# Kernel optimization log

Measured on AMD Instinct MI355X. Metric: run time of the kernel, lower is better.

The kernel has to match this reference:

```python
import jax, jax.numpy as jnp
import numpy as np

N = 2048   # num_nodes
D = 64     # dim
B = 256    # batch of queried nodes
TAU = 1.0


def setup_inputs() -> dict:
    key = jax.random.key(0)
    k_w, k_idx, k_ctx = jax.random.split(key, 3)
    limit = np.sqrt(2.0 / (2 * N)).astype(np.float32)
    W = jax.random.normal(k_w, (N, N, D), dtype=jnp.float32) * limit
    node_indices = jax.random.randint(k_idx, (B,), 0, N, dtype=jnp.int64)
    context_vector = jax.random.normal(k_ctx, (D,), dtype=jnp.float32)
    return {"node_indices": node_indices, "context_vector": context_vector, "W": W}


def reference(node_indices, context_vector, W):
    # Gather per-node weight slabs: (B, N, D)
    w_ij = W[node_indices]
    # Contract against the context vector: (B, N)
    resonance_energy = jnp.einsum('bnd,d->bn', w_ij, context_vector)
    # Temperature-scaled softmax over the node axis
    resonance_scores = jax.nn.softmax(resonance_energy / TAU, axis=-1)
    return resonance_scores
```

## Files before the change

### kernel.cpp

```cpp
#include <hip/hip_runtime.h>
#include <math.h>

#define NN 2048
#define DD 64
#define BB 256
#define BLOCK 1024

#define DPP_ADD(s, ctrl)                                                      \
    s += __int_as_float(__builtin_amdgcn_update_dpp(                          \
        0, __float_as_int(s), (ctrl), 0xf, 0xf, true))

__global__ __launch_bounds__(BLOCK) void resonance_kernel(
    const int* __restrict__ idx,
    const float* __restrict__ ctx,
    const float* __restrict__ W,
    float* __restrict__ out)
{
    const int b    = blockIdx.x;
    const int tid  = threadIdx.x;
    const int lane = tid & 63;
    const int wave = tid >> 6;

    const int node = idx[b];
    const float* __restrict__ Wb = W + (size_t)node * (NN * DD);

    __shared__ float e_lds[NN];
    __shared__ float reds[16];
    __shared__ float bs;

    const float4 c = reinterpret_cast<const float4*>(ctx)[lane & 15];

    float sloc = 0.f;
    #pragma unroll 16
    for (int k = 0; k < NN / 64; ++k) {
        const int n = 4 * (wave + 16 * k) + (lane >> 4);
        const float4 v =
            reinterpret_cast<const float4*>(Wb + (size_t)n * DD)[lane & 15];
        float s = v.x * c.x + v.y * c.y + v.z * c.z + v.w * c.w;
        DPP_ADD(s, 0xB1);
        DPP_ADD(s, 0x4E);
        DPP_ADD(s, 0x141);
        DPP_ADD(s, 0x140);
        const float x = __expf(s);
        sloc += x;
        if ((lane & 15) == 0) e_lds[n] = x;
    }
    sloc += __shfl_xor(sloc, 16);
    sloc += __shfl_xor(sloc, 32);
    if (lane == 0) reds[wave] = sloc;
    __syncthreads();

    if (wave == 0) {
        float t = reds[lane & 15];
        #pragma unroll
        for (int o = 8; o > 0; o >>= 1) t += __shfl_xor(t, o);
        if (lane == 0) bs = t;
    }
    __syncthreads();
    const float inv = 1.0f / bs;

    float* __restrict__ orow = out + (size_t)b * NN;
    orow[tid]         = e_lds[tid] * inv;
    orow[tid + BLOCK] = e_lds[tid + BLOCK] * inv;
}

extern "C" void kernel_launch(void* const* d_in, const int* in_sizes, int n_in,
                              void* d_out, int out_size, void* d_ws, size_t ws_size,
                              hipStream_t stream) {
    const int*   idx = (const int*)d_in[0];
    const float* ctx = (const float*)d_in[1];
    const float* W   = (const float*)d_in[2];
    float*       out = (float*)d_out;

    resonance_kernel<<<BB, BLOCK, 0, stream>>>(idx, ctx, W, out);
}
```

Baseline: 25.20 us.

## Split each query row across eight blocks with a second normalization kernel

The single 1024-thread block per query is replaced by eight 256-thread blocks per query, each handling a 256-row chunk. Each block writes unnormalized exponentials straight to the output and its per-wave partial sums to workspace. A second kernel sums the 32 partials per query and rescales the row in place. This spreads the 32 MB gather across many more blocks than the 256 the GPU had before, at the cost of an extra launch and an extra read-modify-write pass over the output.

```diff
diff --git a/kernel.cpp b/kernel.cpp
--- a/kernel.cpp
+++ b/kernel.cpp
@@ -4,36 +4,40 @@
 #define NN 2048
 #define DD 64
 #define BB 256
-#define BLOCK 1024
+
+#define K1_BLOCKS_PER_Q 8
+#define K1_ROWS (NN / K1_BLOCKS_PER_Q)
+#define K1_BLOCK 256
 
 #define DPP_ADD(s, ctrl)                                                      \
     s += __int_as_float(__builtin_amdgcn_update_dpp(                          \
         0, __float_as_int(s), (ctrl), 0xf, 0xf, true))
 
-__global__ __launch_bounds__(BLOCK) void resonance_kernel(
+__global__ __launch_bounds__(K1_BLOCK, 8) void resonance_k1(
     const int* __restrict__ idx,
     const float* __restrict__ ctx,
     const float* __restrict__ W,
-    float* __restrict__ out)
+    float* __restrict__ out,
+    float* __restrict__ ws)
 {
-    const int b    = blockIdx.x;
-    const int tid  = threadIdx.x;
-    const int lane = tid & 63;
-    const int wave = tid >> 6;
+    const int g     = blockIdx.x;
+    const int b     = g >> 3;
+    const int chunk = (g & 7) * K1_ROWS;
+    const int tid   = threadIdx.x;
+    const int lane  = tid & 63;
+    const int wave  = tid >> 6;
 
     const int node = idx[b];
-    const float* __restrict__ Wb = W + (size_t)node * (NN * DD);
-
-    __shared__ float e_lds[NN];
-    __shared__ float reds[16];
-    __shared__ float bs;
+    const float* __restrict__ Wb =
+        W + (size_t)node * (NN * DD) + (size_t)chunk * DD;
+    float* __restrict__ orow = out + (size_t)b * NN + chunk;
 
     const float4 c = reinterpret_cast<const float4*>(ctx)[lane & 15];
 
     float sloc = 0.f;
-    #pragma unroll 16
-    for (int k = 0; k < NN / 64; ++k) {
-        const int n = 4 * (wave + 16 * k) + (lane >> 4);
+    #pragma unroll 8
+    for (int k = 0; k < K1_ROWS / 16; ++k) {
+        const int n = 4 * (wave + 4 * k) + (lane >> 4);
         const float4 v =
             reinterpret_cast<const float4*>(Wb + (size_t)n * DD)[lane & 15];
         float s = v.x * c.x + v.y * c.y + v.z * c.z + v.w * c.w;
@@ -43,25 +47,32 @@
         DPP_ADD(s, 0x140);
         const float x = __expf(s);
         sloc += x;
-        if ((lane & 15) == 0) e_lds[n] = x;
+        if ((lane & 15) == 0) orow[n] = x;
     }
     sloc += __shfl_xor(sloc, 16);
     sloc += __shfl_xor(sloc, 32);
-    if (lane == 0) reds[wave] = sloc;
-    __syncthreads();
+    if (lane == 0) ws[g * 4 + wave] = sloc;
+}
 
-    if (wave == 0) {
-        float t = reds[lane & 15];
-        #pragma unroll
-        for (int o = 8; o > 0; o >>= 1) t += __shfl_xor(t, o);
-        if (lane == 0) bs = t;
-    }
-    __syncthreads();
-    const float inv = 1.0f / bs;
+__global__ __launch_bounds__(1024) void resonance_k2(
+    float* __restrict__ out,
+    const float* __restrict__ ws)
+{
+    const int b    = blockIdx.x;
+    const int tid  = threadIdx.x;
+    const int lane = tid & 63;
+
+    float t = ws[b * 32 + (lane & 31)];
+    t += __shfl_xor(t, 1);
+    t += __shfl_xor(t, 2);
+    t += __shfl_xor(t, 4);
+    t += __shfl_xor(t, 8);
+    t += __shfl_xor(t, 16);
+    const float inv = 1.0f / t;
 
     float* __restrict__ orow = out + (size_t)b * NN;
-    orow[tid]         = e_lds[tid] * inv;
-    orow[tid + BLOCK] = e_lds[tid + BLOCK] * inv;
+    orow[tid]        *= inv;
+    orow[tid + 1024] *= inv;
 }
 
 extern "C" void kernel_launch(void* const* d_in, const int* in_sizes, int n_in,
@@ -71,6 +82,9 @@
     const float* ctx = (const float*)d_in[1];
     const float* W   = (const float*)d_in[2];
     float*       out = (float*)d_out;
+    float*       ws  = (float*)d_ws;
 
-    resonance_kernel<<<BB, BLOCK, 0, stream>>>(idx, ctx, W, out);
+    resonance_k1<<<BB * K1_BLOCKS_PER_Q, K1_BLOCK, 0, stream>>>(idx, ctx, W,
+                                                                out, ws);
+    resonance_k2<<<BB, 1024, 0, stream>>>(out, ws);
 }
```

New measurement: 26.39 us. 1.05x slower.
